# Kernel optimization log

Measured on AMD Instinct MI355X. Metric: run time of the kernel, lower is better.

The kernel has to match this reference:

```python
import jax, jax.numpy as jnp
import numpy as np

D = 512          # embedding_dim (cfg.hidden_size)
K = 1024         # codebook_size
DECAY = 0.99
EPS = 1e-05
COMMITMENT_COST = 0.25


def setup_inputs() -> dict:
    key = jax.random.key(0)
    k1, k2, k3 = jax.random.split(key, 3)
    return {
        "inputs": jax.random.normal(k1, (32, 1024, D), dtype=jnp.float32),
        "embedding_weight": jax.random.normal(k2, (K, D), dtype=jnp.float32),
        "ema_cluster_size": jnp.zeros((K,), dtype=jnp.float32),
        "ema_w": jax.random.normal(k3, (K, D), dtype=jnp.float32),
    }


def reference(inputs, embedding_weight, ema_cluster_size, ema_w):
    input_shape = inputs.shape
    flat = inputs.reshape(-1, D)  # [N, D]

    # Squared L2 distances to every codebook entry: [N, K]
    distances = (
        jnp.sum(flat ** 2, axis=1, keepdims=True)
        + jnp.sum(embedding_weight ** 2, axis=1)
        - 2.0 * flat @ embedding_weight.T
    )
    idx = jnp.argmin(distances, axis=1)                      # [N]
    encodings = jax.nn.one_hot(idx, K, dtype=flat.dtype)     # [N, K]

    # ---- EMA codebook update (training path) ----
    counts = jnp.sum(encodings, axis=0)                      # == bincount(idx)
    new_cs = ema_cluster_size * DECAY + (1.0 - DECAY) * counts
    n = jnp.sum(new_cs)
    new_cs = (new_cs + EPS) / (n + K * EPS) * n              # Laplace smoothing
    # dw = encodings.T @ flat, done as a fused gather-reduce instead of dense matmul
    dw = jax.ops.segment_sum(flat, idx, num_segments=K)      # [K, D]
    new_ema_w = ema_w * DECAY + (1.0 - DECAY) * dw
    new_embedding = new_ema_w / new_cs[:, None]              # updated codebook

    # quantized = encodings @ new_embedding, expressed as a gather
    quantized = new_embedding[idx].reshape(input_shape)

    e_latent_loss = jnp.mean((jax.lax.stop_gradient(quantized) - inputs) ** 2)
    loss = COMMITMENT_COST * e_latent_loss

    # straight-through estimator
    quantized = inputs + jax.lax.stop_gradient(quantized - inputs)

    avg_probs = jnp.mean(encodings, axis=0)
    perplexity = jnp.exp(-jnp.sum(avg_probs * jnp.log(avg_probs + 1e-10)))
    return (loss, quantized, perplexity, encodings)
```

## Files before the change

kernel.cpp:

```cpp
#include <hip/hip_runtime.h>

#define NROWS 32768
#define DIM   512
#define KC    1024

typedef __attribute__((ext_vector_type(8)))  short short8v;
typedef __attribute__((ext_vector_type(16))) float f32x16;

#define AS1 __attribute__((address_space(1)))
#define AS3 __attribute__((address_space(3)))

__device__ __forceinline__ void split_bf16(float v, short& hi, short& lo) {
    unsigned u = __float_as_uint(v);
    unsigned r = u + 0x7FFFu + ((u >> 16) & 1u);
    hi = (short)(r >> 16);
    float hif = __uint_as_float(r & 0xFFFF0000u);
    float rem = v - hif;
    unsigned u2 = __float_as_uint(rem);
    unsigned r2 = u2 + 0x7FFFu + ((u2 >> 16) & 1u);
    lo = (short)(r2 >> 16);
}

__device__ __forceinline__ void conv8(const float4 a, const float4 b,
                                      short8v& hi, short8v& lo) {
    short h, l;
    split_bf16(a.x, h, l); hi[0] = h; lo[0] = l;
    split_bf16(a.y, h, l); hi[1] = h; lo[1] = l;
    split_bf16(a.z, h, l); hi[2] = h; lo[2] = l;
    split_bf16(a.w, h, l); hi[3] = h; lo[3] = l;
    split_bf16(b.x, h, l); hi[4] = h; lo[4] = l;
    split_bf16(b.y, h, l); hi[5] = h; lo[5] = l;
    split_bf16(b.z, h, l); hi[6] = h; lo[6] = l;
    split_bf16(b.w, h, l); hi[7] = h; lo[7] = l;
}

__device__ __forceinline__ unsigned long long pack_key(float d, int c) {
    unsigned u = __float_as_uint(d);
    u = (u & 0x80000000u) ? ~u : (u | 0x80000000u);
    return ((unsigned long long)u << 32) | (unsigned)c;
}

__global__ __launch_bounds__(256) void k_eprep(const float* __restrict__ E,
                                               short* __restrict__ efrag,
                                               float* __restrict__ en2,
                                               int* __restrict__ counts,
                                               unsigned long long* __restrict__ packed) {
    __shared__ short hbuf[32][520];
    __shared__ short lbuf[32][520];
    int b = blockIdx.x, t = threadIdx.x;
    const float* src = E + (size_t)b * 32 * DIM;
    short* dst = efrag + (size_t)b * 32768;

    unsigned long long* p = packed + b * 1024;
    #pragma unroll
    for (int i = 0; i < 4; ++i) p[t + i * 256] = 0xFFFFFFFFFFFFFFFFull;
    if (b == 0) {
        #pragma unroll
        for (int i = 0; i < 4; ++i) counts[t + i * 256] = 0;
    }

    #pragma unroll
    for (int f = 0; f < 16; ++f) {
        int u = t + f * 256;
        int row = u >> 7, c4 = (u & 127) * 4;
        float4 v = *reinterpret_cast<const float4*>(&src[row * DIM + c4]);
        short4 h4, l4;
        split_bf16(v.x, h4.x, l4.x); split_bf16(v.y, h4.y, l4.y);
        split_bf16(v.z, h4.z, l4.z); split_bf16(v.w, h4.w, l4.w);
        *reinterpret_cast<short4*>(&hbuf[row][c4]) = h4;
        *reinterpret_cast<short4*>(&lbuf[row][c4]) = l4;
    }
    __syncthreads();
    #pragma unroll
    for (int f = 0; f < 16; ++f) {
        int u = t + f * 256;
        int lane = u & 63, h = (u >> 6) & 1, kb = u >> 7;
        int row = lane & 31, k0 = kb * 16 + (lane >> 5) * 8;
        const short* s = h ? &lbuf[row][k0] : &hbuf[row][k0];
        short8v val = *reinterpret_cast<const short8v*>(s);
        *reinterpret_cast<short8v*>(&dst[(size_t)u * 8]) = val;
    }

    int w = t >> 6, lane = t & 63;
    for (int cc = 0; cc < 8; ++cc) {
        int c = b * 32 + w * 8 + cc;
        const float* row = E + (size_t)c * DIM;
        float4 a = *reinterpret_cast<const float4*>(&row[lane * 8]);
        float4 bb = *reinterpret_cast<const float4*>(&row[lane * 8 + 4]);
        float s = a.x*a.x + a.y*a.y + a.z*a.z + a.w*a.w
                + bb.x*bb.x + bb.y*bb.y + bb.z*bb.z + bb.w*bb.w;
        #pragma unroll
        for (int off = 32; off; off >>= 1) s += __shfl_xor(s, off);
        if (!lane) en2[c] = s;
    }
}

__global__ __launch_bounds__(512, 2) void k_argmin(const float* __restrict__ x,
                                                   const short* __restrict__ efrag,
                                                   const float* __restrict__ en2,
                                                   unsigned long long* __restrict__ packed) {
    __shared__ short sA[2][8][2][512];
    __shared__ short sB[3][8][2][512];
    const int tid = threadIdx.x;
    const int w = tid >> 6, l = tid & 63;
    const int wr = w >> 2, wc = w & 3;
    const int l31 = l & 31, lh = l >> 5;

    int bid = blockIdx.x;
    int xcd = bid & 7, j = bid >> 3;
    int row0 = (xcd * 16 + (j >> 2)) * 256;
    int c0   = (j & 3) * 256;

    const float* axsrc = x + (size_t)(row0 + w * 32 + l31) * DIM + lh * 8;
    const short* gsrc = efrag + (size_t)(c0 / 32 + w) * 32768 + l * 8;

    f32x16 acc[4][2];
    #pragma unroll
    for (int a = 0; a < 4; ++a)
        #pragma unroll
        for (int b = 0; b < 2; ++b)
            #pragma unroll
            for (int r = 0; r < 16; ++r) acc[a][b][r] = 0.f;

    float4 ra0, ra1;
    ra0 = *reinterpret_cast<const float4*>(axsrc);
    ra1 = *reinterpret_cast<const float4*>(axsrc + 4);
    __builtin_amdgcn_sched_barrier(0);
    __builtin_amdgcn_global_load_lds((const AS1 void*)gsrc,
                                     (AS3 void*)&sB[0][w][0][0], 16, 0, 0);
    __builtin_amdgcn_global_load_lds((const AS1 void*)(gsrc + 512),
                                     (AS3 void*)&sB[0][w][1][0], 16, 0, 0);
    __builtin_amdgcn_sched_barrier(0);
    asm volatile("s_waitcnt vmcnt(2)" ::: "memory");
    {
        short8v hi, lo; conv8(ra0, ra1, hi, lo);
        *reinterpret_cast<short8v*>(&sA[0][w][0][l * 8]) = hi;
        *reinterpret_cast<short8v*>(&sA[0][w][1][l * 8]) = lo;
    }

    for (int kb = 0; kb < 32; ++kb) {
        const int curA = kb & 1, curB = kb % 3;
        float4 rn0, rn1;
        if (kb < 31) {
            const int nxtA = curA ^ 1, nxtB = (kb + 1) % 3;
            rn0 = *reinterpret_cast<const float4*>(axsrc + (kb + 1) * 16);
            rn1 = *reinterpret_cast<const float4*>(axsrc + (kb + 1) * 16 + 4);
            __builtin_amdgcn_sched_barrier(0);
            __builtin_amdgcn_global_load_lds(
                (const AS1 void*)(gsrc + (size_t)(kb + 1) * 1024),
                (AS3 void*)&sB[nxtB][w][0][0], 16, 0, 0);
            __builtin_amdgcn_global_load_lds(
                (const AS1 void*)(gsrc + (size_t)(kb + 1) * 1024 + 512),
                (AS3 void*)&sB[nxtB][w][1][0], 16, 0, 0);
            __builtin_amdgcn_sched_barrier(0);
            asm volatile("s_waitcnt vmcnt(4) lgkmcnt(0)" ::: "memory");
        } else {
            asm volatile("s_waitcnt vmcnt(0) lgkmcnt(0)" ::: "memory");
        }
        __builtin_amdgcn_s_barrier();
        __builtin_amdgcn_sched_barrier(0);

        {
            short8v ah[4], al[4], bh[2], bl[2];
            const short* pa = &sA[curA][0][0][0];
            const short* pb = &sB[curB][0][0][0];
            #pragma unroll
            for (int m = 0; m < 4; ++m) {
                int g = wr * 4 + m;
                ah[m] = *reinterpret_cast<const short8v*>(pa + (g * 2 + 0) * 512 + l * 8);
                al[m] = *reinterpret_cast<const short8v*>(pa + (g * 2 + 1) * 512 + l * 8);
            }
            #pragma unroll
            for (int n = 0; n < 2; ++n) {
                int g = wc * 2 + n;
                bh[n] = *reinterpret_cast<const short8v*>(pb + (g * 2 + 0) * 512 + l * 8);
                bl[n] = *reinterpret_cast<const short8v*>(pb + (g * 2 + 1) * 512 + l * 8);
            }
            __builtin_amdgcn_s_setprio(1);
            #pragma unroll
            for (int m = 0; m < 4; ++m)
                #pragma unroll
                for (int n = 0; n < 2; ++n) {
                    acc[m][n] = __builtin_amdgcn_mfma_f32_32x32x16_bf16(
                        ah[m], bh[n], acc[m][n], 0, 0, 0);
                    acc[m][n] = __builtin_amdgcn_mfma_f32_32x32x16_bf16(
                        ah[m], bl[n], acc[m][n], 0, 0, 0);
                    acc[m][n] = __builtin_amdgcn_mfma_f32_32x32x16_bf16(
                        al[m], bh[n], acc[m][n], 0, 0, 0);
                }
            __builtin_amdgcn_s_setprio(0);
        }

        if (kb < 31) {
            asm volatile("s_waitcnt vmcnt(2)" ::: "memory");
            short8v hi, lo; conv8(rn0, rn1, hi, lo);
            *reinterpret_cast<short8v*>(&sA[curA ^ 1][w][0][l * 8]) = hi;
            *reinterpret_cast<short8v*>(&sA[curA ^ 1][w][1][l * 8]) = lo;
        }
    }

    float e2[2];
    #pragma unroll
    for (int n = 0; n < 2; ++n) e2[n] = en2[c0 + wc * 64 + n * 32 + l31];
    #pragma unroll
    for (int m = 0; m < 4; ++m) {
        #pragma unroll
        for (int r = 0; r < 16; ++r) {
            unsigned long long key = 0xFFFFFFFFFFFFFFFFull;
            #pragma unroll
            for (int n = 0; n < 2; ++n) {
                float d = fmaf(-2.f, acc[m][n][r], e2[n]);
                unsigned long long k = pack_key(d, c0 + wc * 64 + n * 32 + l31);
                if (k < key) key = k;
            }
            #pragma unroll
            for (int off = 1; off < 32; off <<= 1) {
                unsigned long long o = __shfl_xor(key, off);
                if (o < key) key = o;
            }
            if (l31 == 0) {
                int grow = row0 + wr * 128 + m * 32 + (r & 3) + 8 * (r >> 2) + 4 * lh;
                atomicMin(&packed[grow], key);
            }
        }
    }
}

__global__ __launch_bounds__(256) void k_hist(const unsigned long long* __restrict__ packed,
                                              int* __restrict__ idx,
                                              int* __restrict__ counts) {
    __shared__ int h[KC];
    for (int i = threadIdx.x; i < KC; i += 256) h[i] = 0;
    __syncthreads();
    int g = blockIdx.x * 256 + threadIdx.x;
    int c = (int)(unsigned)(packed[g] & 0xFFFFFFFFull);
    idx[g] = c;
    atomicAdd(&h[c], 1);
    __syncthreads();
    for (int i = threadIdx.x; i < KC; i += 256)
        if (h[i]) atomicAdd(&counts[i], h[i]);
}

__global__ __launch_bounds__(1024) void k_meta(const int* __restrict__ counts,
                                               const float* __restrict__ ema_cs,
                                               float* __restrict__ smoothed,
                                               int* __restrict__ offsets,
                                               int* __restrict__ cursor,
                                               float* __restrict__ perp_out) {
    __shared__ float ws1[16], ws2[16];
    __shared__ int wsum[16];
    int t = threadIdx.x, lane = t & 63, w = t >> 6;
    int cnt = counts[t];
    float cs = ema_cs[t] * 0.99f + 0.01f * (float)cnt;
    float p = (float)cnt / 32768.f;
    float v1 = cs, v2 = p * logf(p + 1e-10f);
    #pragma unroll
    for (int off = 32; off; off >>= 1) {
        v1 += __shfl_xor(v1, off);
        v2 += __shfl_xor(v2, off);
    }
    int s = cnt;
    #pragma unroll
    for (int off = 1; off < 64; off <<= 1) {
        int u = __shfl_up(s, off);
        if (lane >= off) s += u;
    }
    if (lane == 0) { ws1[w] = v1; ws2[w] = v2; }
    if (lane == 63) wsum[w] = s;
    __syncthreads();
    float n = 0.f;
    #pragma unroll
    for (int i = 0; i < 16; ++i) n += ws1[i];
    smoothed[t] = (cs + 1e-5f) / (n + 1024.f * 1e-5f) * n;
    if (t == 0) {
        float sp = 0.f;
        #pragma unroll
        for (int i = 0; i < 16; ++i) sp += ws2[i];
        perp_out[0] = expf(-sp);
    }
    int wo = 0;
    for (int i = 0; i < 16; ++i) if (i < w) wo += wsum[i];
    int off_ = wo + s - cnt;
    offsets[t] = off_;
    cursor[t] = off_;
}

__global__ __launch_bounds__(256) void k_scatter(const int* __restrict__ idx,
                                                 int* __restrict__ cursor,
                                                 int* __restrict__ bucket) {
    int g = blockIdx.x * 256 + threadIdx.x;
    int c = idx[g];
    int pos = atomicAdd(&cursor[c], 1);
    bucket[pos] = g;
}

__global__ __launch_bounds__(256) void k_dw(const float* __restrict__ x,
                                            const float* __restrict__ ema_w,
                                            const int* __restrict__ offsets,
                                            const int* __restrict__ counts,
                                            const int* __restrict__ bucket,
                                            const float* __restrict__ smoothed,
                                            float* __restrict__ newE) {
    __shared__ int rows[256];
    int k = blockIdx.x >> 1, half = blockIdx.x & 1, t = threadIdx.x;
    int d = half * 256 + t;
    int beg = offsets[k], m = counts[k];
    float a = 0.f;
    for (int base = 0; base < m; base += 256) {
        int n = min(256, m - base);
        __syncthreads();
        if (t < n) rows[t] = bucket[beg + base + t];
        __syncthreads();
        int i = 0;
        for (; i + 4 <= n; i += 4) {
            float v0 = x[(size_t)rows[i]     * DIM + d];
            float v1 = x[(size_t)rows[i + 1] * DIM + d];
            float v2 = x[(size_t)rows[i + 2] * DIM + d];
            float v3 = x[(size_t)rows[i + 3] * DIM + d];
            a += v0 + v1 + v2 + v3;
        }
        for (; i < n; ++i) a += x[(size_t)rows[i] * DIM + d];
    }
    newE[(size_t)k * DIM + d] =
        (ema_w[(size_t)k * DIM + d] * 0.99f + 0.01f * a) / smoothed[k];
}

__global__ __launch_bounds__(256) void k_qe(const float* __restrict__ x,
                                            const int* __restrict__ idx,
                                            const float* __restrict__ newE,
                                            float* __restrict__ outq,
                                            float* __restrict__ enc,
                                            float* __restrict__ partials) {
    int b = blockIdx.x, t = threadIdx.x;
    int row8 = b * 8;
    float lp = 0.f;
    #pragma unroll
    for (int it = 0; it < 4; ++it) {
        int slot = t + it * 256;
        int r = slot >> 7;
        int c4 = (slot & 127) * 4;
        int row = row8 + r;
        int code = idx[row];
        float4 in = *reinterpret_cast<const float4*>(&x[(size_t)row * DIM + c4]);
        float4 q  = *reinterpret_cast<const float4*>(&newE[(size_t)code * DIM + c4]);
        float4 d;
        d.x = q.x - in.x; d.y = q.y - in.y; d.z = q.z - in.z; d.w = q.w - in.w;
        float4 o;
        o.x = in.x + d.x; o.y = in.y + d.y; o.z = in.z + d.z; o.w = in.w + d.w;
        *reinterpret_cast<float4*>(&outq[(size_t)row * DIM + c4]) = o;
        lp += d.x*d.x + d.y*d.y + d.z*d.z + d.w*d.w;
    }
    {
        int er = row8 + (t >> 5);
        int l32 = t & 31;
        int one = idx[er];
        float4* dst = reinterpret_cast<float4*>(enc + (size_t)er * KC);
        #pragma unroll
        for (int s = 0; s < 8; ++s) {
            int c4 = l32 + s * 32;
            int base = c4 * 4;
            float4 v;
            v.x = (one == base)     ? 1.f : 0.f;
            v.y = (one == base + 1) ? 1.f : 0.f;
            v.z = (one == base + 2) ? 1.f : 0.f;
            v.w = (one == base + 3) ? 1.f : 0.f;
            dst[c4] = v;
        }
    }
    #pragma unroll
    for (int off = 32; off; off >>= 1) lp += __shfl_xor(lp, off);
    __shared__ float wr[4];
    int lane = t & 63, w = t >> 6;
    if (!lane) wr[w] = lp;
    __syncthreads();
    if (t == 0) partials[b] = wr[0] + wr[1] + wr[2] + wr[3];
}

__global__ __launch_bounds__(256) void k_lossfin(const float* __restrict__ partials,
                                                 float* __restrict__ out0) {
    __shared__ double red[256];
    double s = 0.0;
    for (int i = threadIdx.x; i < 4096; i += 256) s += (double)partials[i];
    red[threadIdx.x] = s; __syncthreads();
    for (int st = 128; st; st >>= 1) {
        if (threadIdx.x < st) red[threadIdx.x] += red[threadIdx.x + st];
        __syncthreads();
    }
    if (!threadIdx.x) out0[0] = (float)(0.25 * red[0] / 16777216.0);
}

extern "C" void kernel_launch(void* const* d_in, const int* in_sizes, int n_in,
                              void* d_out, int out_size, void* d_ws, size_t ws_size,
                              hipStream_t stream) {
    const float* x   = (const float*)d_in[0];
    const float* E   = (const float*)d_in[1];
    const float* ecs = (const float*)d_in[2];
    const float* emw = (const float*)d_in[3];
    float* out = (float*)d_out;

    char* ws = (char*)d_ws;
    int*   idx      = (int*)(ws + 0);
    int*   bucket   = (int*)(ws + 131072);
    float* en2      = (float*)(ws + 262144);
    int*   counts   = (int*)(ws + 266240);
    int*   offsets  = (int*)(ws + 270336);
    int*   cursor   = (int*)(ws + 274432);
    float* smoothed = (float*)(ws + 278528);
    float* newE     = (float*)(ws + 282624);
    float* partials = (float*)(ws + 282624 + 2097152);
    unsigned long long* packed = (unsigned long long*)newE;

    float* out_loss = out;
    float* out_q    = out + 1;
    float* out_perp = out + 16777217;
    float* out_enc  = out + 16777218;

    short* efrag = (short*)out_enc;

    k_eprep  <<<KC / 32, 256, 0, stream>>>(E, efrag, en2, counts, packed);
    k_argmin <<<(NROWS / 256) * 4, 512, 0, stream>>>(x, efrag, en2, packed);
    k_hist   <<<NROWS / 256, 256, 0, stream>>>(packed, idx, counts);
    k_meta   <<<1, 1024, 0, stream>>>(counts, ecs, smoothed, offsets, cursor, out_perp);
    k_scatter<<<NROWS / 256, 256, 0, stream>>>(idx, cursor, bucket);
    k_dw     <<<KC * 2, 256, 0, stream>>>(x, emw, offsets, counts, bucket, smoothed, newE);
    k_qe     <<<NROWS / 8, 256, 0, stream>>>(x, idx, newE, out_q, out_enc, partials);
    k_lossfin<<<1, 256, 0, stream>>>(partials, out_loss);
}
```

Baseline: 315.9 us.

## Use 4-wave blocks with 128x128 per-wave tiles and deeper B prefetch in argmin

The argmin GEMM kernel drops from 8 waves to 4 waves per 256x256 block, so each wave computes a 128x128 tile (4x4 MFMA accumulators) instead of 128x64. Each wave now loads two A and two B fragments per step. The B prefetch is moved two stages ahead, and the barrier now sits after the A conversion. The aim is more MFMA work per LDS fragment read and fewer barrier stalls, at the cost of twice the accumulator registers, lower occupancy (launch bounds 256,1) and fewer waves to hide latency.

Result: slower. 333.2 us (+5.5%).

```diff
diff --git a/kernel.cpp b/kernel.cpp
--- a/kernel.cpp
+++ b/kernel.cpp
@@ -95,7 +95,7 @@
     }
 }
 
-__global__ __launch_bounds__(512, 2) void k_argmin(const float* __restrict__ x,
+__global__ __launch_bounds__(256, 1) void k_argmin(const float* __restrict__ x,
                                                    const short* __restrict__ efrag,
                                                    const float* __restrict__ en2,
                                                    unsigned long long* __restrict__ packed) {
@@ -103,7 +103,7 @@
     __shared__ short sB[3][8][2][512];
     const int tid = threadIdx.x;
     const int w = tid >> 6, l = tid & 63;
-    const int wr = w >> 2, wc = w & 3;
+    const int wr = w >> 1, wc = w & 1;
     const int l31 = l & 31, lh = l >> 5;
 
     int bid = blockIdx.x;
@@ -111,59 +111,83 @@
     int row0 = (xcd * 16 + (j >> 2)) * 256;
     int c0   = (j & 3) * 256;
 
-    const float* axsrc = x + (size_t)(row0 + w * 32 + l31) * DIM + lh * 8;
-    const short* gsrc = efrag + (size_t)(c0 / 32 + w) * 32768 + l * 8;
-
-    f32x16 acc[4][2];
+    const float* axsrc[2];
+    const short* gsrc[2];
+    #pragma unroll
+    for (int g = 0; g < 2; ++g) {
+        axsrc[g] = x + (size_t)(row0 + (w * 2 + g) * 32 + l31) * DIM + lh * 8;
+        gsrc[g]  = efrag + (size_t)(c0 / 32 + w * 2 + g) * 32768 + l * 8;
+    }
+
+    f32x16 acc[4][4];
     #pragma unroll
     for (int a = 0; a < 4; ++a)
         #pragma unroll
-        for (int b = 0; b < 2; ++b)
+        for (int b = 0; b < 4; ++b)
             #pragma unroll
             for (int r = 0; r < 16; ++r) acc[a][b][r] = 0.f;
 
-    float4 ra0, ra1;
-    ra0 = *reinterpret_cast<const float4*>(axsrc);
-    ra1 = *reinterpret_cast<const float4*>(axsrc + 4);
-    __builtin_amdgcn_sched_barrier(0);
-    __builtin_amdgcn_global_load_lds((const AS1 void*)gsrc,
-                                     (AS3 void*)&sB[0][w][0][0], 16, 0, 0);
-    __builtin_amdgcn_global_load_lds((const AS1 void*)(gsrc + 512),
-                                     (AS3 void*)&sB[0][w][1][0], 16, 0, 0);
-    __builtin_amdgcn_sched_barrier(0);
-    asm volatile("s_waitcnt vmcnt(2)" ::: "memory");
     {
-        short8v hi, lo; conv8(ra0, ra1, hi, lo);
-        *reinterpret_cast<short8v*>(&sA[0][w][0][l * 8]) = hi;
-        *reinterpret_cast<short8v*>(&sA[0][w][1][l * 8]) = lo;
+        float4 p0[2], p1[2];
+        #pragma unroll
+        for (int g = 0; g < 2; ++g) {
+            p0[g] = *reinterpret_cast<const float4*>(axsrc[g]);
+            p1[g] = *reinterpret_cast<const float4*>(axsrc[g] + 4);
+        }
+        __builtin_amdgcn_sched_barrier(0);
+        #pragma unroll
+        for (int g = 0; g < 2; ++g) {
+            __builtin_amdgcn_global_load_lds((const AS1 void*)gsrc[g],
+                (AS3 void*)&sB[0][w * 2 + g][0][0], 16, 0, 0);
+            __builtin_amdgcn_global_load_lds((const AS1 void*)(gsrc[g] + 512),
+                (AS3 void*)&sB[0][w * 2 + g][1][0], 16, 0, 0);
+        }
+        #pragma unroll
+        for (int g = 0; g < 2; ++g) {
+            __builtin_amdgcn_global_load_lds((const AS1 void*)(gsrc[g] + 1024),
+                (AS3 void*)&sB[1][w * 2 + g][0][0], 16, 0, 0);
+            __builtin_amdgcn_global_load_lds((const AS1 void*)(gsrc[g] + 1536),
+                (AS3 void*)&sB[1][w * 2 + g][1][0], 16, 0, 0);
+        }
+        #pragma unroll
+        for (int g = 0; g < 2; ++g) {
+            short8v hi, lo; conv8(p0[g], p1[g], hi, lo);
+            *reinterpret_cast<short8v*>(&sA[0][w * 2 + g][0][l * 8]) = hi;
+            *reinterpret_cast<short8v*>(&sA[0][w * 2 + g][1][l * 8]) = lo;
+        }
+        asm volatile("s_waitcnt vmcnt(4) lgkmcnt(0)" ::: "memory");
+        __builtin_amdgcn_s_barrier();
     }
 
     for (int kb = 0; kb < 32; ++kb) {
-        const int curA = kb & 1, curB = kb % 3;
-        float4 rn0, rn1;
+        const int curA = kb & 1;
+        const short* pa = &sA[curA][0][0][0];
+        const short* pb = &sB[kb % 3][0][0][0];
+
+        float4 rn0[2], rn1[2];
         if (kb < 31) {
-            const int nxtA = curA ^ 1, nxtB = (kb + 1) % 3;
-            rn0 = *reinterpret_cast<const float4*>(axsrc + (kb + 1) * 16);
-            rn1 = *reinterpret_cast<const float4*>(axsrc + (kb + 1) * 16 + 4);
+            #pragma unroll
+            for (int g = 0; g < 2; ++g) {
+                rn0[g] = *reinterpret_cast<const float4*>(axsrc[g] + (kb + 1) * 16);
+                rn1[g] = *reinterpret_cast<const float4*>(axsrc[g] + (kb + 1) * 16 + 4);
+            }
             __builtin_amdgcn_sched_barrier(0);
-            __builtin_amdgcn_global_load_lds(
-                (const AS1 void*)(gsrc + (size_t)(kb + 1) * 1024),
-                (AS3 void*)&sB[nxtB][w][0][0], 16, 0, 0);
-            __builtin_amdgcn_global_load_lds(
-                (const AS1 void*)(gsrc + (size_t)(kb + 1) * 1024 + 512),
-                (AS3 void*)&sB[nxtB][w][1][0], 16, 0, 0);
-            __builtin_amdgcn_sched_barrier(0);
-            asm volatile("s_waitcnt vmcnt(4) lgkmcnt(0)" ::: "memory");
-        } else {
-            asm volatile("s_waitcnt vmcnt(0) lgkmcnt(0)" ::: "memory");
-        }
-        __builtin_amdgcn_s_barrier();
-        __builtin_amdgcn_sched_barrier(0);
+        }
+        if (kb < 30) {
+            short* bdst = &sB[(kb + 2) % 3][0][0][0];
+            #pragma unroll
+            for (int g = 0; g < 2; ++g) {
+                __builtin_amdgcn_global_load_lds(
+                    (const AS1 void*)(gsrc[g] + (size_t)(kb + 2) * 1024),
+                    (AS3 void*)(bdst + (w * 2 + g) * 1024), 16, 0, 0);
+                __builtin_amdgcn_global_load_lds(
+                    (const AS1 void*)(gsrc[g] + (size_t)(kb + 2) * 1024 + 512),
+                    (AS3 void*)(bdst + (w * 2 + g) * 1024 + 512), 16, 0, 0);
+            }
+        }
 
         {
-            short8v ah[4], al[4], bh[2], bl[2];
-            const short* pa = &sA[curA][0][0][0];
-            const short* pb = &sB[curB][0][0][0];
+            short8v ah[4], al[4], bh[4], bl[4];
             #pragma unroll
             for (int m = 0; m < 4; ++m) {
                 int g = wr * 4 + m;
@@ -171,8 +195,8 @@
                 al[m] = *reinterpret_cast<const short8v*>(pa + (g * 2 + 1) * 512 + l * 8);
             }
             #pragma unroll
-            for (int n = 0; n < 2; ++n) {
-                int g = wc * 2 + n;
+            for (int n = 0; n < 4; ++n) {
+                int g = wc * 4 + n;
                 bh[n] = *reinterpret_cast<const short8v*>(pb + (g * 2 + 0) * 512 + l * 8);
                 bl[n] = *reinterpret_cast<const short8v*>(pb + (g * 2 + 1) * 512 + l * 8);
             }
@@ -180,37 +204,48 @@
             #pragma unroll
             for (int m = 0; m < 4; ++m)
                 #pragma unroll
-                for (int n = 0; n < 2; ++n) {
+                for (int n = 0; n < 4; ++n)
                     acc[m][n] = __builtin_amdgcn_mfma_f32_32x32x16_bf16(
                         ah[m], bh[n], acc[m][n], 0, 0, 0);
+            #pragma unroll
+            for (int m = 0; m < 4; ++m)
+                #pragma unroll
+                for (int n = 0; n < 4; ++n)
                     acc[m][n] = __builtin_amdgcn_mfma_f32_32x32x16_bf16(
                         ah[m], bl[n], acc[m][n], 0, 0, 0);
+            #pragma unroll
+            for (int m = 0; m < 4; ++m)
+                #pragma unroll
+                for (int n = 0; n < 4; ++n)
                     acc[m][n] = __builtin_amdgcn_mfma_f32_32x32x16_bf16(
                         al[m], bh[n], acc[m][n], 0, 0, 0);
-                }
             __builtin_amdgcn_s_setprio(0);
         }
 
         if (kb < 31) {
-            asm volatile("s_waitcnt vmcnt(2)" ::: "memory");
-            short8v hi, lo; conv8(rn0, rn1, hi, lo);
-            *reinterpret_cast<short8v*>(&sA[curA ^ 1][w][0][l * 8]) = hi;
-            *reinterpret_cast<short8v*>(&sA[curA ^ 1][w][1][l * 8]) = lo;
-        }
-    }
-
-    float e2[2];
-    #pragma unroll
-    for (int n = 0; n < 2; ++n) e2[n] = en2[c0 + wc * 64 + n * 32 + l31];
+            #pragma unroll
+            for (int g = 0; g < 2; ++g) {
+                short8v hi, lo; conv8(rn0[g], rn1[g], hi, lo);
+                *reinterpret_cast<short8v*>(&sA[curA ^ 1][w * 2 + g][0][l * 8]) = hi;
+                *reinterpret_cast<short8v*>(&sA[curA ^ 1][w * 2 + g][1][l * 8]) = lo;
+            }
+            asm volatile("s_waitcnt vmcnt(4) lgkmcnt(0)" ::: "memory");
+            __builtin_amdgcn_s_barrier();
+        }
+    }
+
+    float e2[4];
+    #pragma unroll
+    for (int n = 0; n < 4; ++n) e2[n] = en2[c0 + wc * 128 + n * 32 + l31];
     #pragma unroll
     for (int m = 0; m < 4; ++m) {
         #pragma unroll
         for (int r = 0; r < 16; ++r) {
             unsigned long long key = 0xFFFFFFFFFFFFFFFFull;
             #pragma unroll
-            for (int n = 0; n < 2; ++n) {
+            for (int n = 0; n < 4; ++n) {
                 float d = fmaf(-2.f, acc[m][n][r], e2[n]);
-                unsigned long long k = pack_key(d, c0 + wc * 64 + n * 32 + l31);
+                unsigned long long k = pack_key(d, c0 + wc * 128 + n * 32 + l31);
                 if (k < key) key = k;
             }
             #pragma unroll
@@ -418,7 +453,7 @@
     short* efrag = (short*)out_enc;
 
     k_eprep  <<<KC / 32, 256, 0, stream>>>(E, efrag, en2, counts, packed);
-    k_argmin <<<(NROWS / 256) * 4, 512, 0, stream>>>(x, efrag, en2, packed);
+    k_argmin <<<(NROWS / 256) * 4, 256, 0, stream>>>(x, efrag, en2, packed);
     k_hist   <<<NROWS / 256, 256, 0, stream>>>(packed, idx, counts);
     k_meta   <<<1, 1024, 0, stream>>>(counts, ecs, smoothed, offsets, cursor, out_perp);
     k_scatter<<<NROWS / 256, 256, 0, stream>>>(idx, cursor, bucket);
```
